# Optimization experiments

Hardware: AMD Instinct MI355X
Metric: run time of the kernel (lower is better)

The kernel has to match this reference:

```python
import jax, jax.numpy as jnp
import numpy as np

N_NODES = 50000
N_EDGES = 800000
NUM_RADIAL = 16
HIDDEN = 128


def setup_inputs() -> dict:
    key = jax.random.key(0)
    ks = jax.random.split(key, 9)
    return {
        "x": jax.random.randint(ks[0], (N_NODES,), 0, 100),
        "rbf": jax.random.normal(ks[1], (N_EDGES, NUM_RADIAL), dtype=jnp.float32),
        "i": jax.random.randint(ks[2], (N_EDGES,), 0, N_NODES),
        "j": jax.random.randint(ks[3], (N_EDGES,), 0, N_NODES),
        "emb": jax.random.normal(ks[4], (100, HIDDEN), dtype=jnp.float32),
        "W_rbf": jax.random.normal(ks[5], (HIDDEN, NUM_RADIAL), dtype=jnp.float32) * 0.1,
        "b_rbf": jax.random.normal(ks[6], (HIDDEN,), dtype=jnp.float32) * 0.1,
        "W_lin": jax.random.normal(ks[7], (HIDDEN, 3 * HIDDEN), dtype=jnp.float32) * 0.05,
        "b_lin": jax.random.normal(ks[8], (HIDDEN,), dtype=jnp.float32) * 0.1,
    }


def reference(x, rbf, i, j, emb, W_rbf, b_rbf, W_lin, b_lin):
    # Embed atom types: [N_nodes, H]
    h = emb[x]
    # rbf projection + activation: [E, H]
    r = jax.nn.silu(rbf @ W_rbf.T + b_rbf)
    # Gather endpoints, concat with rbf features: [E, 3H]
    cat = jnp.concatenate([h[i], h[j], r], axis=-1)
    # Final linear + activation: [E, H]
    return jax.nn.silu(cat @ W_lin.T + b_lin)
```

## Files before the change

kernel.cpp:

```cpp
#include <hip/hip_runtime.h>
#include <hip/hip_bf16.h>

#define HID  128
#define NRAD 16
#define NT   100

#define PL_BYTES   (NT * 260 * 2)
#define W3_OFF     PL_BYTES
#define W3_BYTES   (HID * HID * 2)
#define RB_OFF     (W3_OFF + W3_BYTES)
#define LDS_BYTES  (RB_OFF + 8 * 4096)

#define WS_WR_OFF  (PL_BYTES + W3_BYTES)

typedef __attribute__((ext_vector_type(4))) float f32x4;
typedef __attribute__((ext_vector_type(8))) __bf16 bf16x8;
typedef __attribute__((ext_vector_type(4))) __bf16 bf16x4;

union F8 { bf16x8 b; int4 i4; };
union B4 { bf16x4 b4; int2 i2; };

__device__ inline unsigned short f2bfbits(float f){
  unsigned int u = __float_as_uint(f);
  u += 0x7FFFu + ((u >> 16) & 1u);
  return (unsigned short)(u >> 16);
}

__device__ inline float silu_f(float v){
  return v * __builtin_amdgcn_rcpf(1.0f + __expf(-v));
}

__device__ inline float bflo(int q){ return __uint_as_float((unsigned)q << 16); }
__device__ inline float bfhi(int q){ return __uint_as_float((unsigned)q & 0xFFFF0000u); }

__global__ void setup_kernel(const float* __restrict__ emb,
                             const float* __restrict__ W_lin,
                             const float* __restrict__ b_lin,
                             const float* __restrict__ W_rbf,
                             const float* __restrict__ b_rbf,
                             int ntypes,
                             unsigned short* __restrict__ Pbf,
                             char* __restrict__ W3s,
                             unsigned short* __restrict__ Wr32){
  int blk = blockIdx.x;
  int n = threadIdx.x;
  if (blk < ntypes){
    __shared__ float er[HID];
    if (n < HID) er[n] = emb[blk * HID + n];
    __syncthreads();
    int half = n >> 7, nn = n & 127;
    const float4* w4 = (const float4*)(W_lin + (size_t)nn * (3 * HID) + half * HID);
    float s = half ? 0.0f : b_lin[nn];
    #pragma unroll 8
    for (int k4 = 0; k4 < HID / 4; ++k4){
      float4 w = w4[k4];
      s += er[k4*4+0]*w.x + er[k4*4+1]*w.y + er[k4*4+2]*w.z + er[k4*4+3]*w.w;
    }
    Pbf[blk * 260 + n] = f2bfbits(s);
    if (n < 4) Pbf[blk * 260 + 256 + n] = 0;
  } else if (blk < ntypes + 64){
    int idx = (blk - ntypes) * 256 + n;
    int r = idx >> 7, k = idx & 127;
    unsigned short v = f2bfbits(W_lin[(size_t)r * (3 * HID) + 2 * HID + k]);
    int byte = ((r * HID + k) * 2) ^ ((r & 7) << 4);
    *(unsigned short*)(W3s + byte) = v;
  } else {
    int idx = (blk - ntypes - 64) * 256 + n;
    int r = idx >> 5, k = idx & 31;
    float v = (k < 16) ? W_rbf[r * NRAD + k] : (k == 16 ? b_rbf[r] : 0.f);
    Wr32[idx] = f2bfbits(v);
  }
}

__global__ __launch_bounds__(512, 2) void edge_kernel(
    const float* __restrict__ rbf,
    const int*   __restrict__ ei,
    const int*   __restrict__ ej,
    const int*   __restrict__ x,
    const unsigned short* __restrict__ Wr32,
    const int4*  __restrict__ tab,
    float* __restrict__ out,
    int E, int nslab)
{
  extern __shared__ char smem[];

  const int tid  = threadIdx.x;
  const int lane = tid & 63;
  const int wv   = tid >> 6;
  const int erow = lane & 15;
  const int kgrp = lane >> 4;
  char* rbw = smem + RB_OFF + wv * 4096;
  const unsigned short* PlU = (const unsigned short*)smem;
  const char* W3l = smem + W3_OFF;
  const int swz = (erow & 7) << 4;

  for (int i = tid; i < (PL_BYTES + W3_BYTES) / 16; i += 512)
    ((int4*)smem)[i] = tab[i];

  F8 wr[8];
  #pragma unroll
  for (int t = 0; t < 8; ++t)
    wr[t].i4 = *(const int4*)(Wr32 + (t * 16 + erow) * 32 + kgrp * 8);

  const int stride = gridDim.x * 8;
  int slab = blockIdx.x * 8 + wv;

  int xa = 0, xb = 0;
  f32x4 f0 = {0,0,0,0}, f1 = {0,0,0,0};
  if (slab < nslab){
    long ge = (long)slab * 16 + erow; if (ge > (long)E - 1) ge = E - 1;
    xa = x[ei[ge]];
    xb = x[ej[ge]];
    if (kgrp < 2){
      const f32x4* s4 = (const f32x4*)(rbf + ge * NRAD + kgrp * 8);
      f0 = __builtin_nontemporal_load(s4);
      f1 = __builtin_nontemporal_load(s4 + 1);
    }
  }

  __syncthreads();

  while (slab < nslab){
    const long ge   = (long)slab * 16 + erow;
    const int  next = slab + stride;

    int nei = 0, nej = 0;
    f32x4 nf0 = {0,0,0,0}, nf1 = {0,0,0,0};
    if (next < nslab){
      long gn = (long)next * 16 + erow; if (gn > (long)E - 1) gn = E - 1;
      nei = ei[gn];
      nej = ej[gn];
      if (kgrp < 2){
        const f32x4* s4 = (const f32x4*)(rbf + gn * NRAD + kgrp * 8);
        nf0 = __builtin_nontemporal_load(s4);
        nf1 = __builtin_nontemporal_load(s4 + 1);
      }
    }

    F8 fb; fb.i4 = make_int4(0, 0, 0, 0);
    if (kgrp < 2){
      fb.b[0]=(__bf16)f0.x; fb.b[1]=(__bf16)f0.y; fb.b[2]=(__bf16)f0.z; fb.b[3]=(__bf16)f0.w;
      fb.b[4]=(__bf16)f1.x; fb.b[5]=(__bf16)f1.y; fb.b[6]=(__bf16)f1.z; fb.b[7]=(__bf16)f1.w;
    } else if (kgrp == 2){
      fb.b[0] = (__bf16)1.0f;
    }
    #pragma unroll
    for (int t = 0; t < 8; ++t){
      f32x4 acc = {0.f, 0.f, 0.f, 0.f};
      acc = __builtin_amdgcn_mfma_f32_16x16x32_bf16(wr[t].b, fb.b, acc, 0, 0, 0);
      B4 pk;
      pk.b4[0] = (__bf16)silu_f(acc[0]);
      pk.b4[1] = (__bf16)silu_f(acc[1]);
      pk.b4[2] = (__bf16)silu_f(acc[2]);
      pk.b4[3] = (__bf16)silu_f(acc[3]);
      int byte = (erow << 8) + t * 32 + kgrp * 8;
      byte ^= swz;
      *(int2*)(rbw + byte) = pk.i2;
    }

    int nxa = 0, nxb = 0;
    if (next < nslab){ nxa = x[nei]; nxb = x[nej]; }

    asm volatile("s_waitcnt lgkmcnt(0)" ::: "memory");
    __builtin_amdgcn_sched_barrier(0);

    f32x4 acc2[8];
    #pragma unroll
    for (int t = 0; t < 8; ++t) acc2[t] = (f32x4){0.f, 0.f, 0.f, 0.f};

    #pragma unroll
    for (int s = 0; s < 4; ++s){
      int rbyte = ((erow << 8) + s * 64 + kgrp * 16) ^ swz;
      F8 bB; bB.i4 = *(const int4*)(rbw + rbyte);
      #pragma unroll
      for (int t = 0; t < 8; ++t){
        int wbyte = (((t * 16 + erow) << 8) + s * 64 + kgrp * 16) ^ swz;
        F8 aW; aW.i4 = *(const int4*)(W3l + wbyte);
        acc2[t] = __builtin_amdgcn_mfma_f32_16x16x32_bf16(aW.b, bB.b, acc2[t], 0, 0, 0);
      }
    }

    const unsigned short* pa = PlU + xa * 260;
    const unsigned short* pb = PlU + xb * 260 + 128;
    #pragma unroll
    for (int t = 0; t < 8; ++t){
      const int nb = t * 16 + kgrp * 4;
      int2 q1 = *(const int2*)(pa + nb);
      int2 q2 = *(const int2*)(pb + nb);
      f32x4 o;
      o.x = silu_f(acc2[t][0] + bflo(q1.x) + bflo(q2.x));
      o.y = silu_f(acc2[t][1] + bfhi(q1.x) + bfhi(q2.x));
      o.z = silu_f(acc2[t][2] + bflo(q1.y) + bflo(q2.y));
      o.w = silu_f(acc2[t][3] + bfhi(q1.y) + bfhi(q2.y));
      if (ge < E)
        *(f32x4*)(out + ge * HID + nb) = o;
    }

    f0 = nf0; f1 = nf1; xa = nxa; xb = nxb;
    slab = next;
  }
}

extern "C" void kernel_launch(void* const* d_in, const int* in_sizes, int n_in,
                              void* d_out, int out_size, void* d_ws, size_t ws_size,
                              hipStream_t stream){
  const int*   x    = (const int*)  d_in[0];
  const float* rbf  = (const float*)d_in[1];
  const int*   ei   = (const int*)  d_in[2];
  const int*   ej   = (const int*)  d_in[3];
  const float* emb  = (const float*)d_in[4];
  const float* Wrbf = (const float*)d_in[5];
  const float* brbf = (const float*)d_in[6];
  const float* Wlin = (const float*)d_in[7];
  const float* blin = (const float*)d_in[8];
  float* out = (float*)d_out;

  const int E      = in_sizes[2];
  const int ntypes = in_sizes[4] / HID;

  unsigned short* Pbf  = (unsigned short*)d_ws;
  char*           W3s  = (char*)d_ws + PL_BYTES;
  unsigned short* Wr32 = (unsigned short*)((char*)d_ws + WS_WR_OFF);

  setup_kernel<<<ntypes + 64 + 16, 256, 0, stream>>>(
      emb, Wlin, blin, Wrbf, brbf, ntypes, Pbf, W3s, Wr32);

  (void)hipFuncSetAttribute(reinterpret_cast<const void*>(&edge_kernel),
                            hipFuncAttributeMaxDynamicSharedMemorySize, LDS_BYTES);

  const int nslab = (E + 15) / 16;
  edge_kernel<<<256, 512, LDS_BYTES, stream>>>(
      rbf, ei, ej, x, Wr32, (const int4*)d_ws, out, E, nslab);
}
```

Measured before the change: 160.8 us.

## Keep W3 weights in registers, move rbf weights to LDS, store P as fp32

The 128x128 bf16 W3 block now stays in per-lane registers (32 vectors) instead of being read from LDS on every MFMA, and the small rbf projection weights move from registers into a padded LDS table. The per-type precomputed node projections are kept in fp32 in LDS instead of bf16, which removes the unpacking ops and improves accuracy. The aim is to cut LDS traffic in the main GEMM loop. The cost is much higher register pressure under launch_bounds(512,2), which may cause spills, plus a larger P table and the removal of the clamp on prefetched edge indices.

```diff
diff --git a/kernel.cpp b/kernel.cpp
--- a/kernel.cpp
+++ b/kernel.cpp
@@ -5,13 +5,14 @@
 #define NRAD 16
 #define NT   100
 
-#define PL_BYTES   (NT * 260 * 2)
-#define W3_OFF     PL_BYTES
-#define W3_BYTES   (HID * HID * 2)
-#define RB_OFF     (W3_OFF + W3_BYTES)
-#define LDS_BYTES  (RB_OFF + 8 * 4096)
-
-#define WS_WR_OFF  (PL_BYTES + W3_BYTES)
+#define PL_BYTES   (NT * 260 * 4)
+#define RB_OFF     PL_BYTES
+#define WR_OFF     (RB_OFF + 8 * 4096)
+#define WR_BYTES   (HID * 40 * 2)
+#define LDS_BYTES  (WR_OFF + WR_BYTES)
+
+#define WS_W3_OFF  PL_BYTES
+#define WS_WR_OFF  (WS_W3_OFF + HID * HID * 2)
 
 typedef __attribute__((ext_vector_type(4))) float f32x4;
 typedef __attribute__((ext_vector_type(8))) __bf16 bf16x8;
@@ -29,9 +30,6 @@
 __device__ inline float silu_f(float v){
   return v * __builtin_amdgcn_rcpf(1.0f + __expf(-v));
 }
-
-__device__ inline float bflo(int q){ return __uint_as_float((unsigned)q << 16); }
-__device__ inline float bfhi(int q){ return __uint_as_float((unsigned)q & 0xFFFF0000u); }
 
 __global__ void setup_kernel(const float* __restrict__ emb,
                              const float* __restrict__ W_lin,
@@ -39,9 +37,9 @@
                              const float* __restrict__ W_rbf,
                              const float* __restrict__ b_rbf,
                              int ntypes,
-                             unsigned short* __restrict__ Pbf,
-                             char* __restrict__ W3s,
-                             unsigned short* __restrict__ Wr32){
+                             float* __restrict__ P,
+                             unsigned short* __restrict__ W3,
+                             unsigned short* __restrict__ Wr40){
   int blk = blockIdx.x;
   int n = threadIdx.x;
   if (blk < ntypes){
@@ -56,19 +54,17 @@
       float4 w = w4[k4];
       s += er[k4*4+0]*w.x + er[k4*4+1]*w.y + er[k4*4+2]*w.z + er[k4*4+3]*w.w;
     }
-    Pbf[blk * 260 + n] = f2bfbits(s);
-    if (n < 4) Pbf[blk * 260 + 256 + n] = 0;
+    P[blk * 260 + n] = s;
+    if (n < 4) P[blk * 260 + 256 + n] = 0.f;
   } else if (blk < ntypes + 64){
     int idx = (blk - ntypes) * 256 + n;
     int r = idx >> 7, k = idx & 127;
-    unsigned short v = f2bfbits(W_lin[(size_t)r * (3 * HID) + 2 * HID + k]);
-    int byte = ((r * HID + k) * 2) ^ ((r & 7) << 4);
-    *(unsigned short*)(W3s + byte) = v;
+    W3[idx] = f2bfbits(W_lin[(size_t)r * (3 * HID) + 2 * HID + k]);
   } else {
     int idx = (blk - ntypes - 64) * 256 + n;
-    int r = idx >> 5, k = idx & 31;
+    int r = idx / 40, k = idx % 40;
     float v = (k < 16) ? W_rbf[r * NRAD + k] : (k == 16 ? b_rbf[r] : 0.f);
-    Wr32[idx] = f2bfbits(v);
+    Wr40[idx] = f2bfbits(v);
   }
 }
 
@@ -77,12 +73,14 @@
     const int*   __restrict__ ei,
     const int*   __restrict__ ej,
     const int*   __restrict__ x,
-    const unsigned short* __restrict__ Wr32,
-    const int4*  __restrict__ tab,
+    const float* __restrict__ Pg,
+    const unsigned short* __restrict__ W3,
+    const unsigned short* __restrict__ Wr40,
     float* __restrict__ out,
     int E, int nslab)
 {
   extern __shared__ char smem[];
+  const float* Pl = (const float*)smem;
 
   const int tid  = threadIdx.x;
   const int lane = tid & 63;
@@ -90,17 +88,20 @@
   const int erow = lane & 15;
   const int kgrp = lane >> 4;
   char* rbw = smem + RB_OFF + wv * 4096;
-  const unsigned short* PlU = (const unsigned short*)smem;
-  const char* W3l = smem + W3_OFF;
+  const unsigned short* WrL = (const unsigned short*)(smem + WR_OFF);
   const int swz = (erow & 7) << 4;
 
-  for (int i = tid; i < (PL_BYTES + W3_BYTES) / 16; i += 512)
-    ((int4*)smem)[i] = tab[i];
-
-  F8 wr[8];
+  for (int i = tid; i < PL_BYTES / 16; i += 512)
+    ((int4*)smem)[i] = ((const int4*)Pg)[i];
+  for (int i = tid; i < WR_BYTES / 16; i += 512)
+    ((int4*)(smem + WR_OFF))[i] = ((const int4*)Wr40)[i];
+
+  F8 w3r[32];
   #pragma unroll
   for (int t = 0; t < 8; ++t)
-    wr[t].i4 = *(const int4*)(Wr32 + (t * 16 + erow) * 32 + kgrp * 8);
+    #pragma unroll
+    for (int s = 0; s < 4; ++s)
+      w3r[t * 4 + s].i4 = *(const int4*)(W3 + (t * 16 + erow) * HID + s * 32 + kgrp * 8);
 
   const int stride = gridDim.x * 8;
   int slab = blockIdx.x * 8 + wv;
@@ -127,7 +128,7 @@
     int nei = 0, nej = 0;
     f32x4 nf0 = {0,0,0,0}, nf1 = {0,0,0,0};
     if (next < nslab){
-      long gn = (long)next * 16 + erow; if (gn > (long)E - 1) gn = E - 1;
+      long gn = (long)next * 16 + erow;
       nei = ei[gn];
       nej = ej[gn];
       if (kgrp < 2){
@@ -146,8 +147,9 @@
     }
     #pragma unroll
     for (int t = 0; t < 8; ++t){
+      F8 fa; fa.i4 = *(const int4*)(WrL + (t * 16 + erow) * 40 + kgrp * 8);
       f32x4 acc = {0.f, 0.f, 0.f, 0.f};
-      acc = __builtin_amdgcn_mfma_f32_16x16x32_bf16(wr[t].b, fb.b, acc, 0, 0, 0);
+      acc = __builtin_amdgcn_mfma_f32_16x16x32_bf16(fa.b, fb.b, acc, 0, 0, 0);
       B4 pk;
       pk.b4[0] = (__bf16)silu_f(acc[0]);
       pk.b4[1] = (__bf16)silu_f(acc[1]);
@@ -173,25 +175,22 @@
       int rbyte = ((erow << 8) + s * 64 + kgrp * 16) ^ swz;
       F8 bB; bB.i4 = *(const int4*)(rbw + rbyte);
       #pragma unroll
-      for (int t = 0; t < 8; ++t){
-        int wbyte = (((t * 16 + erow) << 8) + s * 64 + kgrp * 16) ^ swz;
-        F8 aW; aW.i4 = *(const int4*)(W3l + wbyte);
-        acc2[t] = __builtin_amdgcn_mfma_f32_16x16x32_bf16(aW.b, bB.b, acc2[t], 0, 0, 0);
-      }
-    }
-
-    const unsigned short* pa = PlU + xa * 260;
-    const unsigned short* pb = PlU + xb * 260 + 128;
+      for (int t = 0; t < 8; ++t)
+        acc2[t] = __builtin_amdgcn_mfma_f32_16x16x32_bf16(w3r[t*4+s].b, bB.b, acc2[t], 0, 0, 0);
+    }
+
+    const float* pa = Pl + xa * 260;
+    const float* pb = Pl + xb * 260 + 128;
     #pragma unroll
     for (int t = 0; t < 8; ++t){
       const int nb = t * 16 + kgrp * 4;
-      int2 q1 = *(const int2*)(pa + nb);
-      int2 q2 = *(const int2*)(pb + nb);
+      f32x4 p1 = *(const f32x4*)(pa + nb);
+      f32x4 p2 = *(const f32x4*)(pb + nb);
       f32x4 o;
-      o.x = silu_f(acc2[t][0] + bflo(q1.x) + bflo(q2.x));
-      o.y = silu_f(acc2[t][1] + bfhi(q1.x) + bfhi(q2.x));
-      o.z = silu_f(acc2[t][2] + bflo(q1.y) + bflo(q2.y));
-      o.w = silu_f(acc2[t][3] + bfhi(q1.y) + bfhi(q2.y));
+      o.x = silu_f(acc2[t][0] + p1.x + p2.x);
+      o.y = silu_f(acc2[t][1] + p1.y + p2.y);
+      o.z = silu_f(acc2[t][2] + p1.z + p2.z);
+      o.w = silu_f(acc2[t][3] + p1.w + p2.w);
       if (ge < E)
         *(f32x4*)(out + ge * HID + nb) = o;
     }
@@ -218,17 +217,17 @@
   const int E      = in_sizes[2];
   const int ntypes = in_sizes[4] / HID;
 
-  unsigned short* Pbf  = (unsigned short*)d_ws;
-  char*           W3s  = (char*)d_ws + PL_BYTES;
-  unsigned short* Wr32 = (unsigned short*)((char*)d_ws + WS_WR_OFF);
-
-  setup_kernel<<<ntypes + 64 + 16, 256, 0, stream>>>(
-      emb, Wlin, blin, Wrbf, brbf, ntypes, Pbf, W3s, Wr32);
+  float*          P    = (float*)d_ws;
+  unsigned short* W3   = (unsigned short*)((char*)d_ws + WS_W3_OFF);
+  unsigned short* Wr40 = (unsigned short*)((char*)d_ws + WS_WR_OFF);
+
+  setup_kernel<<<ntypes + 64 + 20, 256, 0, stream>>>(
+      emb, Wlin, blin, Wrbf, brbf, ntypes, P, W3, Wr40);
 
   (void)hipFuncSetAttribute(reinterpret_cast<const void*>(&edge_kernel),
                             hipFuncAttributeMaxDynamicSharedMemorySize, LDS_BYTES);
 
   const int nslab = (E + 15) / 16;
   edge_kernel<<<256, 512, LDS_BYTES, stream>>>(
-      rbf, ei, ej, x, Wr32, (const int4*)d_ws, out, E, nslab);
-}
+      rbf, ei, ej, x, P, W3, Wr40, out, E, nslab);
+}
```

Result: slower. 166.2 us (+3.4%).
